# Kernel tuning notes

Hardware: AMD Instinct MI355X
Metric: run time of the kernel (lower is better)

The kernel has to match this reference:

```python
import jax, jax.numpy as jnp
import numpy as np

B, T, C, H, TT = 8, 1024, 512, 8, 4  # batch, seq, n_embd, n_head, total_timestep
D = C // H


def setup_inputs() -> dict:
    key = jax.random.key(0)
    ks = jax.random.split(key, 4)
    s = 1.0 / np.sqrt(C)
    return {
        "x": jax.random.normal(ks[0], (B, T, C), jnp.float32),
        "padding_mask": jax.random.bernoulli(ks[1], 0.1, (TT, T)),  # bool
        "W_qkv": jax.random.normal(ks[2], (C, 3 * C), jnp.float32) * s,
        "b_qkv": jnp.zeros((3 * C,), jnp.float32),
        "W_proj": jax.random.normal(ks[3], (C, C), jnp.float32) * s,
        "b_proj": jnp.zeros((C,), jnp.float32),
    }


def reference(x, padding_mask, W_qkv, b_qkv, W_proj, b_proj):
    # fused QKV projection
    qkv = x @ W_qkv + b_qkv                       # [B,T,3C]
    q, k, v = jnp.split(qkv, 3, axis=-1)
    q = q.reshape(B, T, H, D)
    k = k.reshape(B, T, H, D)
    v = v.reshape(B, T, H, D)

    # mask: causal OR padding (True = attend), replicating torch semantics
    causal = jnp.tril(jnp.ones((T, T), bool))                 # [T,T]
    m = causal[None] | padding_mask[:, :, None]               # [TT,T,T]
    mask = jnp.broadcast_to(m[None], (B // TT, TT, T, T)).reshape(B, 1, T, T)

    scores = jnp.einsum("bqhd,bkhd->bhqk", q, k) * (1.0 / np.sqrt(D))
    scores = jnp.where(mask, scores, jnp.float32(-1e30))
    attn = jax.nn.softmax(scores, axis=-1)                    # [B,H,T,T]
    y = jnp.einsum("bhqk,bkhd->bqhd", attn, v).reshape(B, T, C)
    return y @ W_proj + b_proj
```

## Files before the change

kernel.cpp:

```cpp
#include <hip/hip_runtime.h>
#include <hip/hip_bf16.h>

#define BB 8
#define TT_ 4
#define TSEQ 1024
#define CEMB 512
#define NH 8
#define HD 64

typedef __attribute__((ext_vector_type(8))) short bf16x8;
typedef __attribute__((ext_vector_type(4))) float f32x4;
typedef __attribute__((ext_vector_type(16))) float f32x16;

#define AS1 __attribute__((address_space(1)))
#define AS3 __attribute__((address_space(3)))

__device__ __forceinline__ void gload_lds16(const void* g, void* l) {
  __builtin_amdgcn_global_load_lds((const AS1 unsigned int*)g, (AS3 unsigned int*)l, 16, 0, 0);
}

__device__ __forceinline__ short f2b(float f) {
  union { float f; unsigned u; } v; v.f = f;
  unsigned r = v.u + 0x7FFFu + ((v.u >> 16) & 1u);
  return (short)(r >> 16);
}

__device__ __forceinline__ unsigned pack2(float a, float b) {
  unsigned r;
  asm("v_cvt_pk_bf16_f32 %0, %1, %2" : "=v"(r) : "v"(a), "v"(b));
  return r;
}

__global__ __launch_bounds__(256) void k_prep(
    const float* __restrict__ x, short* __restrict__ xb,
    const float* __restrict__ w0, short* __restrict__ t0,
    const float* __restrict__ w1, short* __restrict__ t1,
    const void* __restrict__ pin, int* __restrict__ pme,
    int* __restrict__ perm, int* __restrict__ chunk_nkt)
{
  __shared__ float tsh[64][65];
  const int bid = blockIdx.x;

  if (bid < 2048) {
    const int i = bid * 256 + threadIdx.x;
    float4 v0 = ((const float4*)x)[i * 2];
    float4 v1 = ((const float4*)x)[i * 2 + 1];
    union { unsigned u[4]; bf16x8 v; } o;
    o.u[0] = pack2(v0.x, v0.y); o.u[1] = pack2(v0.z, v0.w);
    o.u[2] = pack2(v1.x, v1.y); o.u[3] = pack2(v1.z, v1.w);
    ((bf16x8*)xb)[i] = o.v;
    return;
  }

  if (bid < 2304) {
    const int z = (bid >= 2240);
    const int tile = z ? (bid - 2240) : (bid - 2048);
    const int ntx = z ? 8 : 24;
    const float* w = z ? w1 : w0;
    short* wt = z ? t1 : t0;
    const int N = z ? 512 : 1536, K = 512;
    const int tx = threadIdx.x & 15, ty = threadIdx.x >> 4;
    const int n0 = (tile % ntx) * 64, k0 = (tile / ntx) * 64;
#pragma unroll
    for (int i = 0; i < 4; ++i) {
      int kr = i * 16 + ty;
      float4 v = *(const float4*)&w[(size_t)(k0 + kr) * N + n0 + tx * 4];
      tsh[tx * 4 + 0][kr] = v.x; tsh[tx * 4 + 1][kr] = v.y;
      tsh[tx * 4 + 2][kr] = v.z; tsh[tx * 4 + 3][kr] = v.w;
    }
    __syncthreads();
#pragma unroll
    for (int i = 0; i < 4; ++i) {
      int nr = i * 16 + ty;
      short4 o;
      o.x = f2b(tsh[nr][tx * 4 + 0]); o.y = f2b(tsh[nr][tx * 4 + 1]);
      o.z = f2b(tsh[nr][tx * 4 + 2]); o.w = f2b(tsh[nr][tx * 4 + 3]);
      *(short4*)&wt[(size_t)(n0 + nr) * K + k0 + tx * 4] = o;
    }
    return;
  }

  __shared__ int bad_f32, any_f32, bad_i32, any_i32, bad_u16, any_u16;
  if (threadIdx.x == 0) { bad_f32 = any_f32 = bad_i32 = any_i32 = bad_u16 = any_u16 = 0; }
  __syncthreads();
  const unsigned char* pb = (const unsigned char*)pin;
  const float* pf = (const float*)pin;
  const int* pi = (const int*)pin;
  const unsigned short* ph = (const unsigned short*)pin;
  for (int i = threadIdx.x; i < 1024; i += 256) {
    float fv = pf[i];
    if (fv != 0.0f && fv != 1.0f) bad_f32 = 1;
    if (fv == 1.0f) any_f32 = 1;
    int iv = pi[i];
    if (iv != 0 && iv != 1) bad_i32 = 1;
    if (iv == 1) any_i32 = 1;
  }
  for (int i = threadIdx.x; i < 2048; i += 256) {
    unsigned short hv = ph[i];
    if (hv != 0 && hv != 0x3F80u && hv != 0x3C00u) bad_u16 = 1;
    if (hv == 0x3F80u || hv == 0x3C00u) any_u16 = 1;
  }
  __syncthreads();
  int mode = 3;
  if (!bad_f32 && any_f32) mode = 0;
  else if (!bad_i32 && any_i32) mode = 1;
  else if (!bad_u16 && any_u16) mode = 2;
  for (int i = threadIdx.x; i < TT_ * TSEQ; i += 256) {
    int v;
    if (mode == 0)      v = (pf[i] != 0.0f);
    else if (mode == 1) v = (pi[i] != 0);
    else if (mode == 2) v = (ph[i] != 0);
    else                v = (pb[i] != 0);
    pme[i] = v;
  }
  __syncthreads();

  const int w = threadIdx.x >> 6, lane = threadIdx.x & 63;
  {
    const int* rowp = pme + w * 1024;
    unsigned long long bal[16];
    int npm = 0;
#pragma unroll
    for (int g = 0; g < 16; ++g) {
      bal[g] = __ballot(rowp[g * 64 + lane] != 0);
      npm += __popcll(bal[g]);
    }
    int off_non = 0, off_pm = 1024 - npm;
#pragma unroll
    for (int g = 0; g < 16; ++g) {
      unsigned long long m = bal[g];
      int below = __popcll(m & ((1ull << lane) - 1ull));
      int ispm = (int)((m >> lane) & 1ull);
      int pos = ispm ? (off_pm + below) : (off_non + lane - below);
      perm[w * 1024 + pos] = g * 64 + lane;
      int c = __popcll(m);
      off_pm += c; off_non += 64 - c;
    }
  }
  __syncthreads();
  {
    const int tt = w, c = (lane >> 3) & 7, seg = lane & 7;
    int mx = 0;
#pragma unroll
    for (int i = 0; i < 16; ++i) {
      int q = perm[tt * 1024 + c * 128 + seg * 16 + i];
      int need = pme[tt * 1024 + q] ? 16 : ((q >> 6) + 1);
      mx = mx > need ? mx : need;
    }
#pragma unroll
    for (int s = 1; s < 8; s <<= 1) {
      int o = __shfl_xor(mx, s, 64);
      mx = mx > o ? mx : o;
    }
    if (seg == 0) chunk_nkt[tt * 8 + c] = mx;
  }
}

template<int MODE, int NT>
__global__ __launch_bounds__(256) void k_gemm(
    const short* __restrict__ A, const short* __restrict__ Bt,
    const float* __restrict__ bias,
    short* __restrict__ qb, short* __restrict__ kb, short* __restrict__ vtb,
    float* __restrict__ fout)
{
  __shared__ short As[2][128 * 32];
  __shared__ short Bs[2][128 * 32];
  const int tid = threadIdx.x, lane = tid & 63, w = tid >> 6;
  const int wm = w >> 1, wn = w & 1;
  const int idp = (blockIdx.x & 7) * ((NT * 64) >> 3) + (blockIdx.x >> 3);
  const int n0 = (idp % NT) * 128, m0 = (idp / NT) * 128;
  f32x4 acc[4][4] = {};
  const char* Abase = (const char*)A + (size_t)m0 * 1024;
  const char* Bbase = (const char*)Bt + (size_t)n0 * 1024;
  const int rowL = w * 16 + (lane >> 2);
  const int colB = (lane & 3) * 16;

  auto stage = [&](int buf, int k0) {
#pragma unroll
    for (int is = 0; is < 2; ++is) {
      int row = is * 64 + rowL;
      gload_lds16(Abase + (size_t)row * 1024 + (size_t)(k0 * 2 + colB),
                  (char*)As[buf] + is * 4096 + w * 1024);
      gload_lds16(Bbase + (size_t)row * 1024 + (size_t)(k0 * 2 + colB),
                  (char*)Bs[buf] + is * 4096 + w * 1024);
    }
  };

  stage(0, 0);
  __syncthreads();
  int buf = 0;
  for (int k0 = 0; k0 < 512; k0 += 32) {
    if (k0 + 32 < 512) stage(buf ^ 1, k0 + 32);
    bf16x8 a[4], bfr[4];
#pragma unroll
    for (int mf = 0; mf < 4; ++mf)
      a[mf] = *(const bf16x8*)&As[buf][(wm * 64 + mf * 16 + (lane & 15)) * 32 + (lane >> 4) * 8];
#pragma unroll
    for (int nf = 0; nf < 4; ++nf)
      bfr[nf] = *(const bf16x8*)&Bs[buf][(wn * 64 + nf * 16 + (lane & 15)) * 32 + (lane >> 4) * 8];
#pragma unroll
    for (int mf = 0; mf < 4; ++mf)
#pragma unroll
      for (int nf = 0; nf < 4; ++nf)
        acc[mf][nf] = __builtin_amdgcn_mfma_f32_16x16x32_bf16(a[mf], bfr[nf], acc[mf][nf], 0, 0, 0);
    __syncthreads();
    buf ^= 1;
  }

#pragma unroll
  for (int nf = 0; nf < 4; ++nf) {
    const int n_g = n0 + wn * 64 + nf * 16 + (lane & 15);
    const float bv = bias[n_g];
    if (MODE == 0) {
      const int which = n_g >> 9;
      const int c = n_g & 511;
      const int h = c >> 6, d = c & 63;
      const float qsc = (which == 0) ? 0.18033688011112043f : 1.0f;
#pragma unroll
      for (int mf = 0; mf < 4; ++mf) {
        const int mb = m0 + wm * 64 + mf * 16 + ((lane >> 4) << 2);
        const int b = mb >> 10, t0 = mb & 1023;
        const int b8h = b * NH + h;
        if (which == 2) {
          short4 pk;
          pk.x = f2b(acc[mf][nf][0] + bv);
          pk.y = f2b(acc[mf][nf][1] + bv);
          pk.z = f2b(acc[mf][nf][2] + bv);
          pk.w = f2b(acc[mf][nf][3] + bv);
          *(short4*)&vtb[((size_t)b8h * HD + d) * TSEQ + t0] = pk;
        } else {
          short* dst = (which == 0) ? qb : kb;
          size_t base = ((size_t)b8h * TSEQ + t0) * HD + d;
#pragma unroll
          for (int r = 0; r < 4; ++r)
            dst[base + (size_t)r * HD] = f2b((acc[mf][nf][r] + bv) * qsc);
        }
      }
    } else {
#pragma unroll
      for (int mf = 0; mf < 4; ++mf) {
        const int mb = m0 + wm * 64 + mf * 16 + ((lane >> 4) << 2);
#pragma unroll
        for (int r = 0; r < 4; ++r)
          fout[(size_t)(mb + r) * 512 + n_g] = acc[mf][nf][r] + bv;
      }
    }
  }
}

__device__ __forceinline__ void pv_step(
    f32x16 p, int sub, int hi, int lq, const char* Vsb, f32x16& o0, f32x16& o1)
{
  unsigned P2[8];
#pragma unroll
  for (int i = 0; i < 8; ++i) P2[i] = pack2(p[2 * i], p[2 * i + 1]);
  unsigned e0 = __shfl_xor(hi ? P2[0] : P2[2], 32, 64);
  unsigned e1 = __shfl_xor(hi ? P2[1] : P2[3], 32, 64);
  unsigned e2 = __shfl_xor(hi ? P2[4] : P2[6], 32, 64);
  unsigned e3 = __shfl_xor(hi ? P2[5] : P2[7], 32, 64);
  union { unsigned u[4]; bf16x8 v; } f0, f1;
  f0.u[0] = hi ? e0 : P2[0]; f0.u[1] = hi ? e1 : P2[1];
  f0.u[2] = hi ? P2[2] : e0; f0.u[3] = hi ? P2[3] : e1;
  f1.u[0] = hi ? e2 : P2[4]; f1.u[1] = hi ? e3 : P2[5];
  f1.u[2] = hi ? P2[6] : e2; f1.u[3] = hi ? P2[7] : e3;
  __builtin_amdgcn_s_setprio(1);
#pragma unroll
  for (int dt = 0; dt < 2; ++dt) {
    int row = dt * 32 + lq;
    bf16x8 v0 = *(const bf16x8*)(Vsb + row * 128 + ((4 * sub + hi) ^ (row & 7)) * 16);
    bf16x8 v1 = *(const bf16x8*)(Vsb + row * 128 + ((4 * sub + 2 + hi) ^ (row & 7)) * 16);
    f32x16& o = dt ? o1 : o0;
    o = __builtin_amdgcn_mfma_f32_32x32x16_bf16(v0, f0.v, o, 0, 0, 0);
    o = __builtin_amdgcn_mfma_f32_32x32x16_bf16(v1, f1.v, o, 0, 0, 0);
  }
  __builtin_amdgcn_s_setprio(0);
}

__global__ __launch_bounds__(512) void k_attn(
    const short* __restrict__ qg, const short* __restrict__ kg,
    const short* __restrict__ vtg, const int* __restrict__ pme,
    const int* __restrict__ perm, const int* __restrict__ chunk_nkt,
    short* __restrict__ yb)
{
  __shared__ char smem[65536];
  const int tid = threadIdx.x, lane = tid & 63, w = tid >> 6;
  const int g = w >> 2;
  const int hi = lane >> 5, lq = lane & 31;
  const int id = blockIdx.x;
  const int bh = id & 63, b = bh >> 3, h = bh & 7, tt = b & 3;
  const int chunk = 7 - (id >> 6);
  const char* Qb = (const char*)(qg + (size_t)bh * TSEQ * HD);
  const char* Kb = (const char*)(kg + (size_t)bh * TSEQ * HD);
  const char* Vb = (const char*)(vtg + (size_t)bh * HD * TSEQ);

  const int stg_row = ((w & 3) << 3) + (lane >> 3);
  const int stg_cl = (lane & 7) ^ ((lane >> 3) & 7);

  auto stage = [&](int buf, int kt) {
#pragma unroll
    for (int is = 0; is < 2; ++is) {
      int row = is * 32 + stg_row;
      gload_lds16(Kb + (size_t)(kt * 64 + row) * 128 + stg_cl * 16,
                  smem + buf * 8192 + is * 4096 + (w & 3) * 1024);
      gload_lds16(Vb + (size_t)row * 2048 + kt * 128 + stg_cl * 16,
                  smem + 32768 + buf * 8192 + is * 4096 + (w & 3) * 1024);
    }
  };

  const int nkt = chunk_nkt[tt * 8 + chunk];
  const int q_g = perm[tt * 1024 + chunk * 128 + (w & 3) * 32 + lq];
  const int pmrow = pme[tt * TSEQ + q_g];

  if (g < nkt) stage(g * 2, g);

  int wmq = q_g, wnq = q_g;
#pragma unroll
  for (int s = 1; s < 64; s <<= 1) {
    wmq = max(wmq, __shfl_xor(wmq, s, 64));
    wnq = min(wnq, __shfl_xor(wnq, s, 64));
  }
  const int whaspm = __any(pmrow != 0);

  bf16x8 qf[4];
#pragma unroll
  for (int dk = 0; dk < 4; ++dk)
    qf[dk] = *(const bf16x8*)(Qb + (size_t)q_g * 128 + dk * 32 + hi * 16);

  float mrun = -1e30f, lrun = 0.0f;
  f32x16 o0 = {}, o1 = {};

  const int niter = (nkt + 1) >> 1;
  for (int i = 0; i < niter; ++i) {
    asm volatile("s_waitcnt vmcnt(0)" ::: "memory");
    __builtin_amdgcn_s_barrier();
    const int kt = 2 * i + g;
    if (kt + 2 < nkt) stage(g * 2 + ((i + 1) & 1), kt + 2);

    const int kb_ = kt * 64;
    if (kt < nkt && (kb_ <= wmq || whaspm)) {
      const char* Ksb = smem + (g * 2 + (i & 1)) * 8192;
      const char* Vsb = smem + 32768 + (g * 2 + (i & 1)) * 8192;

      f32x16 s0 = {}, s1 = {};
      __builtin_amdgcn_s_setprio(1);
#pragma unroll
      for (int dk = 0; dk < 4; ++dk) {
        int row0 = lq, row1 = 32 + lq;
        bf16x8 kf0 = *(const bf16x8*)(Ksb + row0 * 128 + ((2 * dk + hi) ^ (row0 & 7)) * 16);
        bf16x8 kf1 = *(const bf16x8*)(Ksb + row1 * 128 + ((2 * dk + hi) ^ (row1 & 7)) * 16);
        s0 = __builtin_amdgcn_mfma_f32_32x32x16_bf16(kf0, qf[dk], s0, 0, 0, 0);
        s1 = __builtin_amdgcn_mfma_f32_32x32x16_bf16(kf1, qf[dk], s1, 0, 0, 0);
      }
      __builtin_amdgcn_s_setprio(0);

      if (kb_ + 63 <= wnq) {
      } else if (kb_ > wmq) {
#pragma unroll
        for (int r = 0; r < 16; ++r) {
          s0[r] = pmrow ? s0[r] : -1e30f;
          s1[r] = pmrow ? s1[r] : -1e30f;
        }
      } else {
#pragma unroll
        for (int r = 0; r < 16; ++r) {
          int crow = (r & 3) + 8 * (r >> 2) + 4 * hi;
          s0[r] = ((kb_ + crow <= q_g) || pmrow) ? s0[r] : -1e30f;
          s1[r] = ((kb_ + 32 + crow <= q_g) || pmrow) ? s1[r] : -1e30f;
        }
      }

      float tm[16];
#pragma unroll
      for (int r = 0; r < 16; ++r) tm[r] = fmaxf(s0[r], s1[r]);
#pragma unroll
      for (int st = 8; st >= 1; st >>= 1)
#pragma unroll
        for (int r = 0; r < 8; ++r)
          if (r < st) tm[r] = fmaxf(tm[r], tm[r + st]);
      float mx = fmaxf(tm[0], __shfl_xor(tm[0], 32, 64));
      if (!__all(mx <= mrun + 8.0f)) {
        float nm = fmaxf(mrun, mx);
        float sc = __builtin_amdgcn_exp2f(mrun - nm);
        lrun *= sc;
#pragma unroll
        for (int r = 0; r < 16; ++r) { o0[r] *= sc; o1[r] *= sc; }
        mrun = nm;
      }
#pragma unroll
      for (int r = 0; r < 16; ++r) s0[r] = __builtin_amdgcn_exp2f(s0[r] - mrun);
#pragma unroll
      for (int r = 0; r < 16; ++r) s1[r] = __builtin_amdgcn_exp2f(s1[r] - mrun);
      float ts[16];
#pragma unroll
      for (int r = 0; r < 16; ++r) ts[r] = s0[r] + s1[r];
#pragma unroll
      for (int st = 8; st >= 1; st >>= 1)
#pragma unroll
        for (int r = 0; r < 8; ++r)
          if (r < st) ts[r] = ts[r] + ts[r + st];
      lrun += ts[0] + __shfl_xor(ts[0], 32, 64);

      pv_step(s0, 0, hi, lq, Vsb, o0, o1);
      pv_step(s1, 1, hi, lq, Vsb, o0, o1);
    }
  }

  __syncthreads();
  float* mg = (float*)smem;
  const int idx = (w & 3) * 64 + lane;
  if (g == 1) {
    mg[idx * 34 + 0] = mrun;
    mg[idx * 34 + 1] = lrun;
#pragma unroll
    for (int j = 0; j < 16; ++j) mg[idx * 34 + 2 + j] = o0[j];
#pragma unroll
    for (int j = 0; j < 16; ++j) mg[idx * 34 + 18 + j] = o1[j];
  }
  __syncthreads();
  if (g == 0) {
    const float mB = mg[idx * 34 + 0], lB = mg[idx * 34 + 1];
    const float m = fmaxf(mrun, mB);
    const float wa = __builtin_amdgcn_exp2f(mrun - m);
    const float wb = __builtin_amdgcn_exp2f(mB - m);
    const float linv = 1.0f / (lrun * wa + lB * wb);
    const float fa = wa * linv, fb = wb * linv;
    short* yrow = yb + ((size_t)b * TSEQ + q_g) * CEMB + h * HD;
#pragma unroll
    for (int dt = 0; dt < 2; ++dt) {
      const f32x16& o = dt ? o1 : o0;
      const int ob = dt ? 18 : 2;
#pragma unroll
      for (int gg = 0; gg < 4; ++gg) {
        short4 pk;
        pk.x = f2b(o[4 * gg + 0] * fa + mg[idx * 34 + ob + 4 * gg + 0] * fb);
        pk.y = f2b(o[4 * gg + 1] * fa + mg[idx * 34 + ob + 4 * gg + 1] * fb);
        pk.z = f2b(o[4 * gg + 2] * fa + mg[idx * 34 + ob + 4 * gg + 2] * fb);
        pk.w = f2b(o[4 * gg + 3] * fa + mg[idx * 34 + ob + 4 * gg + 3] * fb);
        *(short4*)(yrow + dt * 32 + 8 * gg + 4 * hi) = pk;
      }
    }
  }
}

extern "C" void kernel_launch(void* const* d_in, const int* in_sizes, int n_in,
                              void* d_out, int out_size, void* d_ws, size_t ws_size,
                              hipStream_t stream) {
  const float* x     = (const float*)d_in[0];
  const void*  pmask = d_in[1];
  const float* Wqkv  = (const float*)d_in[2];
  const float* bqkv  = (const float*)d_in[3];
  const float* Wproj = (const float*)d_in[4];
  const float* bproj = (const float*)d_in[5];
  float* out = (float*)d_out;
  char* ws = (char*)d_ws;

  const size_t OFF_XB   = 0;
  const size_t OFF_WQT  = 8388608;
  const size_t OFF_WPT  = 9961472;
  const size_t OFF_Q    = 10485760;
  const size_t OFF_K    = 18874368;
  const size_t OFF_VT   = 27262976;
  const size_t OFF_Y    = 35651584;
  const size_t OFF_PM   = 44040192;
  const size_t OFF_PERM = 44056576;
  const size_t OFF_CNKT = 44072960;
  const size_t NEED     = 44073984;
  if (ws_size < NEED) return;

  short* xb  = (short*)(ws + OFF_XB);
  short* wqT = (short*)(ws + OFF_WQT);
  short* wpT = (short*)(ws + OFF_WPT);
  short* qb  = (short*)(ws + OFF_Q);
  short* kb  = (short*)(ws + OFF_K);
  short* vtb = (short*)(ws + OFF_VT);
  short* yb  = (short*)(ws + OFF_Y);
  int*   pme = (int*)(ws + OFF_PM);
  int*   prm = (int*)(ws + OFF_PERM);
  int*   cnk = (int*)(ws + OFF_CNKT);

  k_prep<<<dim3(2305), dim3(256), 0, stream>>>(x, xb, Wqkv, wqT, Wproj, wpT,
                                               pmask, pme, prm, cnk);
  k_gemm<0, 12><<<dim3(768), dim3(256), 0, stream>>>(xb, wqT, bqkv, qb, kb, vtb, nullptr);
  k_attn<<<dim3(512), dim3(512), 0, stream>>>(qb, kb, vtb, pme, prm, cnk, yb);
  k_gemm<1, 4><<<dim3(256), dim3(256), 0, stream>>>(yb, wpT, bproj, nullptr, nullptr, nullptr, out);
}
```

Measured before the change: 84.21 us.

## Read K/V tiles directly from global memory and use per-wave tile counts

Removes the double-buffered LDS staging of K and V tiles (global_load_lds plus block barriers), so MFMA operands are loaded straight from global memory through the cache. Each wave now computes its own number of key tiles from its max query index and padding flag instead of a per-chunk count, which lets waves finish independently. This removes the barrier synchronisation and cuts LDS use to just the merge buffer, which may raise occupancy. The cost is uncoalesced, higher-latency global loads in the inner loop and redundant K/V reads across the four waves of each group.

```diff
diff --git a/kernel.cpp b/kernel.cpp
--- a/kernel.cpp
+++ b/kernel.cpp
@@ -249,7 +249,7 @@
 }
 
 __device__ __forceinline__ void pv_step(
-    f32x16 p, int sub, int hi, int lq, const char* Vsb, f32x16& o0, f32x16& o1)
+    f32x16 p, int sub, int hi, int lq, const char* Vtile, f32x16& o0, f32x16& o1)
 {
   unsigned P2[8];
 #pragma unroll
@@ -267,8 +267,8 @@
 #pragma unroll
   for (int dt = 0; dt < 2; ++dt) {
     int row = dt * 32 + lq;
-    bf16x8 v0 = *(const bf16x8*)(Vsb + row * 128 + ((4 * sub + hi) ^ (row & 7)) * 16);
-    bf16x8 v1 = *(const bf16x8*)(Vsb + row * 128 + ((4 * sub + 2 + hi) ^ (row & 7)) * 16);
+    bf16x8 v0 = *(const bf16x8*)(Vtile + (size_t)row * 2048 + (4 * sub + hi) * 16);
+    bf16x8 v1 = *(const bf16x8*)(Vtile + (size_t)row * 2048 + (4 * sub + 2 + hi) * 16);
     f32x16& o = dt ? o1 : o0;
     o = __builtin_amdgcn_mfma_f32_32x32x16_bf16(v0, f0.v, o, 0, 0, 0);
     o = __builtin_amdgcn_mfma_f32_32x32x16_bf16(v1, f1.v, o, 0, 0, 0);
@@ -279,10 +279,9 @@
 __global__ __launch_bounds__(512) void k_attn(
     const short* __restrict__ qg, const short* __restrict__ kg,
     const short* __restrict__ vtg, const int* __restrict__ pme,
-    const int* __restrict__ perm, const int* __restrict__ chunk_nkt,
-    short* __restrict__ yb)
+    const int* __restrict__ perm, short* __restrict__ yb)
 {
-  __shared__ char smem[65536];
+  __shared__ float mg[256 * 34];
   const int tid = threadIdx.x, lane = tid & 63, w = tid >> 6;
   const int g = w >> 2;
   const int hi = lane >> 5, lq = lane & 31;
@@ -293,25 +292,8 @@
   const char* Kb = (const char*)(kg + (size_t)bh * TSEQ * HD);
   const char* Vb = (const char*)(vtg + (size_t)bh * HD * TSEQ);
 
-  const int stg_row = ((w & 3) << 3) + (lane >> 3);
-  const int stg_cl = (lane & 7) ^ ((lane >> 3) & 7);
-
-  auto stage = [&](int buf, int kt) {
-#pragma unroll
-    for (int is = 0; is < 2; ++is) {
-      int row = is * 32 + stg_row;
-      gload_lds16(Kb + (size_t)(kt * 64 + row) * 128 + stg_cl * 16,
-                  smem + buf * 8192 + is * 4096 + (w & 3) * 1024);
-      gload_lds16(Vb + (size_t)row * 2048 + kt * 128 + stg_cl * 16,
-                  smem + 32768 + buf * 8192 + is * 4096 + (w & 3) * 1024);
-    }
-  };
-
-  const int nkt = chunk_nkt[tt * 8 + chunk];
   const int q_g = perm[tt * 1024 + chunk * 128 + (w & 3) * 32 + lq];
   const int pmrow = pme[tt * TSEQ + q_g];
-
-  if (g < nkt) stage(g * 2, g);
 
   int wmq = q_g, wnq = q_g;
 #pragma unroll
@@ -320,6 +302,7 @@
     wnq = min(wnq, __shfl_xor(wnq, s, 64));
   }
   const int whaspm = __any(pmrow != 0);
+  const int wave_nkt = whaspm ? (TSEQ / 64) : ((wmq >> 6) + 1);
 
   bf16x8 qf[4];
 #pragma unroll
@@ -329,84 +312,74 @@
   float mrun = -1e30f, lrun = 0.0f;
   f32x16 o0 = {}, o1 = {};
 
-  const int niter = (nkt + 1) >> 1;
-  for (int i = 0; i < niter; ++i) {
-    asm volatile("s_waitcnt vmcnt(0)" ::: "memory");
-    __builtin_amdgcn_s_barrier();
-    const int kt = 2 * i + g;
-    if (kt + 2 < nkt) stage(g * 2 + ((i + 1) & 1), kt + 2);
-
+  for (int kt = g; kt < wave_nkt; kt += 2) {
     const int kb_ = kt * 64;
-    if (kt < nkt && (kb_ <= wmq || whaspm)) {
-      const char* Ksb = smem + (g * 2 + (i & 1)) * 8192;
-      const char* Vsb = smem + 32768 + (g * 2 + (i & 1)) * 8192;
-
-      f32x16 s0 = {}, s1 = {};
-      __builtin_amdgcn_s_setprio(1);
-#pragma unroll
-      for (int dk = 0; dk < 4; ++dk) {
-        int row0 = lq, row1 = 32 + lq;
-        bf16x8 kf0 = *(const bf16x8*)(Ksb + row0 * 128 + ((2 * dk + hi) ^ (row0 & 7)) * 16);
-        bf16x8 kf1 = *(const bf16x8*)(Ksb + row1 * 128 + ((2 * dk + hi) ^ (row1 & 7)) * 16);
-        s0 = __builtin_amdgcn_mfma_f32_32x32x16_bf16(kf0, qf[dk], s0, 0, 0, 0);
-        s1 = __builtin_amdgcn_mfma_f32_32x32x16_bf16(kf1, qf[dk], s1, 0, 0, 0);
+    const char* Ktile = Kb + (size_t)kb_ * 128;
+    const char* Vtile = Vb + (size_t)kt * 128;
+
+    f32x16 s0 = {}, s1 = {};
+    __builtin_amdgcn_s_setprio(1);
+#pragma unroll
+    for (int dk = 0; dk < 4; ++dk) {
+      bf16x8 kf0 = *(const bf16x8*)(Ktile + (size_t)lq * 128 + (2 * dk + hi) * 16);
+      bf16x8 kf1 = *(const bf16x8*)(Ktile + (size_t)(32 + lq) * 128 + (2 * dk + hi) * 16);
+      s0 = __builtin_amdgcn_mfma_f32_32x32x16_bf16(kf0, qf[dk], s0, 0, 0, 0);
+      s1 = __builtin_amdgcn_mfma_f32_32x32x16_bf16(kf1, qf[dk], s1, 0, 0, 0);
+    }
+    __builtin_amdgcn_s_setprio(0);
+
+    if (kb_ + 63 <= wnq) {
+    } else if (kb_ > wmq) {
+#pragma unroll
+      for (int r = 0; r < 16; ++r) {
+        s0[r] = pmrow ? s0[r] : -1e30f;
+        s1[r] = pmrow ? s1[r] : -1e30f;
       }
-      __builtin_amdgcn_s_setprio(0);
-
-      if (kb_ + 63 <= wnq) {
-      } else if (kb_ > wmq) {
-#pragma unroll
-        for (int r = 0; r < 16; ++r) {
-          s0[r] = pmrow ? s0[r] : -1e30f;
-          s1[r] = pmrow ? s1[r] : -1e30f;
-        }
-      } else {
-#pragma unroll
-        for (int r = 0; r < 16; ++r) {
-          int crow = (r & 3) + 8 * (r >> 2) + 4 * hi;
-          s0[r] = ((kb_ + crow <= q_g) || pmrow) ? s0[r] : -1e30f;
-          s1[r] = ((kb_ + 32 + crow <= q_g) || pmrow) ? s1[r] : -1e30f;
-        }
+    } else {
+#pragma unroll
+      for (int r = 0; r < 16; ++r) {
+        int crow = (r & 3) + 8 * (r >> 2) + 4 * hi;
+        s0[r] = ((kb_ + crow <= q_g) || pmrow) ? s0[r] : -1e30f;
+        s1[r] = ((kb_ + 32 + crow <= q_g) || pmrow) ? s1[r] : -1e30f;
       }
-
-      float tm[16];
-#pragma unroll
-      for (int r = 0; r < 16; ++r) tm[r] = fmaxf(s0[r], s1[r]);
-#pragma unroll
-      for (int st = 8; st >= 1; st >>= 1)
-#pragma unroll
-        for (int r = 0; r < 8; ++r)
-          if (r < st) tm[r] = fmaxf(tm[r], tm[r + st]);
-      float mx = fmaxf(tm[0], __shfl_xor(tm[0], 32, 64));
-      if (!__all(mx <= mrun + 8.0f)) {
-        float nm = fmaxf(mrun, mx);
-        float sc = __builtin_amdgcn_exp2f(mrun - nm);
-        lrun *= sc;
-#pragma unroll
-        for (int r = 0; r < 16; ++r) { o0[r] *= sc; o1[r] *= sc; }
-        mrun = nm;
-      }
-#pragma unroll
-      for (int r = 0; r < 16; ++r) s0[r] = __builtin_amdgcn_exp2f(s0[r] - mrun);
-#pragma unroll
-      for (int r = 0; r < 16; ++r) s1[r] = __builtin_amdgcn_exp2f(s1[r] - mrun);
-      float ts[16];
-#pragma unroll
-      for (int r = 0; r < 16; ++r) ts[r] = s0[r] + s1[r];
-#pragma unroll
-      for (int st = 8; st >= 1; st >>= 1)
-#pragma unroll
-        for (int r = 0; r < 8; ++r)
-          if (r < st) ts[r] = ts[r] + ts[r + st];
-      lrun += ts[0] + __shfl_xor(ts[0], 32, 64);
-
-      pv_step(s0, 0, hi, lq, Vsb, o0, o1);
-      pv_step(s1, 1, hi, lq, Vsb, o0, o1);
-    }
-  }
-
-  __syncthreads();
-  float* mg = (float*)smem;
+    }
+
+    float tm[16];
+#pragma unroll
+    for (int r = 0; r < 16; ++r) tm[r] = fmaxf(s0[r], s1[r]);
+#pragma unroll
+    for (int st = 8; st >= 1; st >>= 1)
+#pragma unroll
+      for (int r = 0; r < 8; ++r)
+        if (r < st) tm[r] = fmaxf(tm[r], tm[r + st]);
+    float mx = fmaxf(tm[0], __shfl_xor(tm[0], 32, 64));
+    if (!__all(mx <= mrun + 8.0f)) {
+      float nm = fmaxf(mrun, mx);
+      float sc = __builtin_amdgcn_exp2f(mrun - nm);
+      lrun *= sc;
+#pragma unroll
+      for (int r = 0; r < 16; ++r) { o0[r] *= sc; o1[r] *= sc; }
+      mrun = nm;
+    }
+#pragma unroll
+    for (int r = 0; r < 16; ++r) s0[r] = __builtin_amdgcn_exp2f(s0[r] - mrun);
+#pragma unroll
+    for (int r = 0; r < 16; ++r) s1[r] = __builtin_amdgcn_exp2f(s1[r] - mrun);
+    float ts[16];
+#pragma unroll
+    for (int r = 0; r < 16; ++r) ts[r] = s0[r] + s1[r];
+#pragma unroll
+    for (int st = 8; st >= 1; st >>= 1)
+#pragma unroll
+      for (int r = 0; r < 8; ++r)
+        if (r < st) ts[r] = ts[r] + ts[r + st];
+    lrun += ts[0] + __shfl_xor(ts[0], 32, 64);
+
+    pv_step(s0, 0, hi, lq, Vtile, o0, o1);
+    pv_step(s1, 1, hi, lq, Vtile, o0, o1);
+  }
+
+  __syncthreads();
   const int idx = (w & 3) * 64 + lane;
   if (g == 1) {
     mg[idx * 34 + 0] = mrun;
@@ -481,6 +454,6 @@
   k_prep<<<dim3(2305), dim3(256), 0, stream>>>(x, xb, Wqkv, wqT, Wproj, wpT,
                                                pmask, pme, prm, cnk);
   k_gemm<0, 12><<<dim3(768), dim3(256), 0, stream>>>(xb, wqT, bqkv, qb, kb, vtb, nullptr);
-  k_attn<<<dim3(512), dim3(512), 0, stream>>>(qb, kb, vtb, pme, prm, cnk, yb);
+  k_attn<<<dim3(512), dim3(512), 0, stream>>>(qb, kb, vtb, pme, prm, yb);
   k_gemm<1, 4><<<dim3(256), dim3(256), 0, stream>>>(yb, wpT, bproj, nullptr, nullptr, nullptr, out);
 }
```

Measured after the change: 105.5 us. +25.3%, slower.
